# Kernel optimization log

Measured on AMD Instinct MI355X. Metric: run time of the kernel, lower is better.

## Reference

```python
import jax, jax.numpy as jnp
import numpy as np

DT = 0.1  # source sets dt = 0.1 globally
B, XS, SS, H = 128, 64, 16, 512  # batch, x_size, s_size, hidden_size


def setup_inputs() -> dict:
    key = jax.random.key(0)
    ks = jax.random.split(key, 14)
    sc = 1.0 / np.sqrt(H)  # PyTorch LSTM/Linear init bound
    u = lambda k, shape: jax.random.uniform(k, shape, jnp.float32, -sc, sc)
    return {
        "x": jax.random.normal(ks[0], (B, XS), jnp.float32),
        "s0": jax.random.normal(ks[1], (B, SS), jnp.float32),
        # LSTM layer 0 (input = x_size + s_size), gate order i,f,g,o
        "W_ih0": u(ks[2], (4 * H, XS + SS)),
        "W_hh0": u(ks[3], (4 * H, H)),
        "b_ih0": u(ks[4], (4 * H,)),
        "b_hh0": u(ks[5], (4 * H,)),
        # LSTM layer 1 (input = hidden)
        "W_ih1": u(ks[6], (4 * H, H)),
        "W_hh1": u(ks[7], (4 * H, H)),
        "b_ih1": u(ks[8], (4 * H,)),
        "b_hh1": u(ks[9], (4 * H,)),
        # fc: hidden -> s_size
        "W_fc": u(ks[10], (SS, H)),
        "b_fc": u(ks[11], (SS,)),
        "max_time": 20,
    }


def _lstm_cell(h, c, inp, W_ih, W_hh, b_ih, b_hh):
    g = inp @ W_ih.T + b_ih + h @ W_hh.T + b_hh  # [B, 4H]
    i, f, gg, o = jnp.split(g, 4, axis=-1)  # torch gate order i,f,g,o
    c = jax.nn.sigmoid(f) * c + jax.nn.sigmoid(i) * jnp.tanh(gg)
    h = jax.nn.sigmoid(o) * jnp.tanh(c)
    return h, c


def reference(x, s0, W_ih0, W_hh0, b_ih0, b_hh0, W_ih1, W_hh1, b_ih1, b_hh1, W_fc, b_fc, max_time):
    T = int(max_time / DT) + 1  # while cal_t <= max_time, cal_t += dt
    batch = x.shape[0]
    hid = W_hh0.shape[1]
    zeros = jnp.zeros((batch, hid), x.dtype)
    init = (zeros, zeros, zeros, zeros, s0)  # (h0,c0,h1,c1,current_s)

    def step(carry, _):
        h0, c0, h1, c1, s = carry
        inp = jnp.concatenate([x, s], axis=-1)  # [B, XS+SS]
        h0, c0 = _lstm_cell(h0, c0, inp, W_ih0, W_hh0, b_ih0, b_hh0)
        h1, c1 = _lstm_cell(h1, c1, h0, W_ih1, W_hh1, b_ih1, b_hh1)
        step_out = h1 @ W_fc.T + b_fc  # [B, SS] (dropout is identity in eval)
        s = s + step_out * DT  # residual Euler update
        return (h0, c0, h1, c1, s), (s, step_out)

    _, (outs, res) = jax.lax.scan(step, init, None, length=T)
    outputs = jnp.transpose(outs, (1, 0, 2))  # [B, T, SS]
    res_steps = jnp.transpose(res, (1, 0, 2))  # [B, T, SS]
    cal_times = jnp.arange(T, dtype=x.dtype) * DT
    return outputs, cal_times, res_steps
```

## Files before the change

### kernel.cpp

```cpp
#include <hip/hip_runtime.h>

#define NB    256
#define BT    1024
#define BATCH 128
#define HID   512
#define XSZ   64
#define SSZ   16
#define CPAD  32
#define SPIN_MAX (1 << 17)

typedef unsigned int uint;
typedef unsigned long long ulong64;
typedef _Float16 half2v __attribute__((ext_vector_type(2)));

#define AL8(p)    __hip_atomic_load((const ulong64*)(p), __ATOMIC_RELAXED, __HIP_MEMORY_SCOPE_AGENT)
#define AS4(p, v) __hip_atomic_store((uint*)(p), (v), __ATOMIC_RELAXED, __HIP_MEMORY_SCOPE_AGENT)

__device__ __align__(16) uint4 g_h0Q[2][64 * 128];
__device__ __align__(16) uint4 g_h1Q[2][64 * 128];
__device__ __align__(16) float g_Wcomb[4 * HID * HID];
__device__ int g_cnt[512 * CPAD];

__device__ __forceinline__ float sigf(float x) { return 1.f / (1.f + __expf(-x)); }
__device__ __forceinline__ float tanh_fast(float x) {
  float ax = fabsf(x); float e = __expf(-2.f * ax);
  return copysignf((1.f - e) / (1.f + e), x);
}
__device__ __forceinline__ uint pack_f16(float a, float b) {
  half2v h; h.x = (_Float16)a; h.y = (_Float16)b;
  return __builtin_bit_cast(uint, h);
}
__device__ __forceinline__ float2 up2(uint u) {
  half2v h = __builtin_bit_cast(half2v, u);
  return make_float2((float)h.x, (float)h.y);
}
__device__ __forceinline__ float fdot2(uint a, uint w, float c) {
#if __has_builtin(__builtin_amdgcn_fdot2)
  return __builtin_amdgcn_fdot2(__builtin_bit_cast(half2v, a),
                                __builtin_bit_cast(half2v, w), c, false);
#else
  float2 av = up2(a), wv = up2(w);
  return fmaf(av.x, wv.x, fmaf(av.y, wv.y, c));
#endif
}
__device__ __forceinline__ void dot8(uint a, uint4 w0, uint4 w1, float* acc) {
  acc[0] = fdot2(a, w0.x, acc[0]); acc[1] = fdot2(a, w0.y, acc[1]);
  acc[2] = fdot2(a, w0.z, acc[2]); acc[3] = fdot2(a, w0.w, acc[3]);
  acc[4] = fdot2(a, w1.x, acc[4]); acc[5] = fdot2(a, w1.y, acc[5]);
  acc[6] = fdot2(a, w1.z, acc[6]); acc[7] = fdot2(a, w1.w, acc[7]);
}
__device__ __forceinline__ void dots16(const uint4* __restrict__ apq,
                                       const uint*  __restrict__ wb,
                                       float* __restrict__ acc) {
  const ulong64* ap = (const ulong64*)apq;
  ulong64 lo[16], hi[16];
#pragma unroll
  for (int i = 0; i < 16; ++i) {
    lo[i] = AL8(ap + i * 256);
    hi[i] = AL8(ap + i * 256 + 1);
  }
#pragma unroll
  for (int i = 0; i < 16; ++i) {
    const uint4* w4 = (const uint4*)(wb + 32 * i);
    dot8((uint)lo[i],         w4[0], w4[1], acc);
    dot8((uint)(lo[i] >> 32), w4[2], w4[3], acc);
    dot8((uint)hi[i],         w4[4], w4[5], acc);
    dot8((uint)(hi[i] >> 32), w4[6], w4[7], acc);
  }
}

__device__ __forceinline__ void cnt_wait(int pid) {
  int guard = 0;
  while (__hip_atomic_load(&g_cnt[pid * CPAD], __ATOMIC_RELAXED, __HIP_MEMORY_SCOPE_AGENT) < NB) {
    __builtin_amdgcn_s_sleep(2);
    if (++guard > SPIN_MAX) break;
  }
  __builtin_amdgcn_sched_barrier(0);
}

__device__ __forceinline__ void group_wait(int pid, int pw, int tid, int* rel) {
  if ((tid >> 6) == pw) {
    cnt_wait(pid);
    if ((tid & 63) == 0)
      __hip_atomic_store(&rel[pid & 1], pid, __ATOMIC_RELEASE, __HIP_MEMORY_SCOPE_WORKGROUP);
  } else {
    int guard = 0;
    while (__hip_atomic_load(&rel[pid & 1], __ATOMIC_ACQUIRE, __HIP_MEMORY_SCOPE_WORKGROUP) < pid) {
      __builtin_amdgcn_s_sleep(1);
      if (++guard > SPIN_MAX) break;
    }
    __builtin_amdgcn_sched_barrier(0);
  }
}

__global__ void setup_kernel(float* __restrict__ out, int T) {
  int idx = blockIdx.x * blockDim.x + threadIdx.x;
  int n   = gridDim.x * blockDim.x;
  uint* z0 = (uint*)g_h0Q;
  uint* z1 = (uint*)g_h1Q;
  for (int i = idx; i < 2 * 64 * 128 * 4; i += n) { z0[i] = 0u; z1[i] = 0u; }
  for (int t = idx; t < T; t += n) out[BATCH * T * SSZ + t] = (float)t * 0.1f;
  for (int i = idx; i < 512 * CPAD; i += n) g_cnt[i] = 0;
}

__global__ void wcomb_kernel(const float* __restrict__ Wih0, const float* __restrict__ Wfc) {
  int idx = blockIdx.x * blockDim.x + threadIdx.x;
  int row = idx >> 9, k = idx & (HID - 1);
  float a = 0.f;
#pragma unroll
  for (int m = 0; m < SSZ; m++) a += Wih0[row * (XSZ + SSZ) + XSZ + m] * Wfc[m * HID + k];
  g_Wcomb[idx] = 0.1f * a;
}

__global__ __launch_bounds__(BT, 4) void persist_kernel(
    const float* __restrict__ x,    const float* __restrict__ s0,
    const float* __restrict__ Wih0, const float* __restrict__ Whh0,
    const float* __restrict__ bih0, const float* __restrict__ bhh0,
    const float* __restrict__ Wih1, const float* __restrict__ Whh1,
    const float* __restrict__ bih1, const float* __restrict__ bhh1,
    const float* __restrict__ Wfc,  const float* __restrict__ bfc,
    float* __restrict__ out, int T)
{
  __shared__ uint  lwT[4][256][8];
  __shared__ float gbuf[8][8][128];
  __shared__ float sbase[8][128];
  __shared__ float c0s[2][128], c1s[2][128];
  __shared__ uint  wfcP[16][268];
  __shared__ float b1s[8], ucs[8];
  __shared__ int   rel[2];

  const int bk  = blockIdx.x;
  const int tid = threadIdx.x;
  const int ks  = tid >> 7;
  const int b   = tid & 127;
  const int q0  = (ks & 3) * 16;
  const int kp0 = (ks & 3) * 64;

  if (tid == 0) { rel[0] = -1; rel[1] = -1; }

  for (int e = tid; e < 4 * 256 * 8; e += BT) {
    int mat = e >> 11, kp = (e >> 3) & 255, r = e & 7;
    int row = (r >> 1) * HID + 2 * bk + (r & 1);
    const float* src = (mat == 0) ? &Whh0[row * HID]
                     : (mat == 1) ? &g_Wcomb[row * HID]
                     : (mat == 2) ? &Wih1[row * HID] : &Whh1[row * HID];
    lwT[mat][kp][r] = pack_f16(src[2 * kp], src[2 * kp + 1]);
  }
  for (int e = tid; e < 16 * 256; e += BT) {
    int fs_ = e >> 8, kp = e & 255;
    wfcP[fs_][kp] = pack_f16(Wfc[fs_ * HID + 2 * kp], Wfc[fs_ * HID + 2 * kp + 1]);
  }
  {
    int r = tid >> 7, bb = tid & 127;
    int row = (r >> 1) * HID + 2 * bk + (r & 1);
    float a = bih0[row] + bhh0[row];
    const float* wr = Wih0 + row * (XSZ + SSZ);
#pragma unroll 4
    for (int k = 0; k < XSZ; k++) a = fmaf(wr[k], x[bb * XSZ + k], a);
    sbase[r][bb] = a;
  }
  if (tid < 8) {
    int row = (tid >> 1) * HID + 2 * bk + (tid & 1);
    b1s[tid] = bih1[row] + bhh1[row];
    float uc = 0.f;
    const float* ws = Wih0 + row * (XSZ + SSZ) + XSZ;
#pragma unroll
    for (int m = 0; m < SSZ; m++) uc = fmaf(ws[m], bfc[m], uc);
    ucs[tid] = 0.1f * uc;
  }
  __syncthreads();

  float u[8];
  if (tid < 128) {
#pragma unroll
    for (int r = 0; r < 8; r++) {
      int row = (r >> 1) * HID + 2 * bk + (r & 1);
      const float* ws = Wih0 + row * (XSZ + SSZ) + XSZ;
      float a = 0.f;
#pragma unroll
      for (int m = 0; m < SSZ; m++) a = fmaf(ws[m], s0[b * SSZ + m], a);
      u[r] = a - ucs[r];
    }
    c0s[0][b] = 0.f; c0s[1][b] = 0.f;
    c1s[0][b] = 0.f; c1s[1][b] = 0.f;
  }

  const bool fcw = (bk >= 128) && ((tid >> 6) == 15);
  const int  fb = bk - 128, lane = tid & 63, fs = lane & 15, fq = lane >> 4;
  float s_reg = 0.f, bfcj = 0.f;
  if (fcw && lane < SSZ) { s_reg = s0[fb * SSZ + lane]; bfcj = bfc[lane]; }

  auto fc_step = [&](int tt, const uint4* h1base) {
    const ulong64* hp = (const ulong64*)(h1base + fq * 16 * 128 + fb);
    ulong64 lo[16], hi[16];
#pragma unroll
    for (int i = 0; i < 16; ++i) {
      lo[i] = AL8(hp + i * 256);
      hi[i] = AL8(hp + i * 256 + 1);
    }
    const uint4* wp = (const uint4*)&wfcP[fs][fq * 64];
    float acc = 0.f;
#pragma unroll
    for (int i = 0; i < 16; ++i) {
      uint4 w = wp[i];
      acc = fdot2((uint)lo[i],         w.x, acc);
      acc = fdot2((uint)(lo[i] >> 32), w.y, acc);
      acc = fdot2((uint)hi[i],         w.z, acc);
      acc = fdot2((uint)(hi[i] >> 32), w.w, acc);
    }
    acc += __shfl_xor(acc, 16);
    acc += __shfl_xor(acc, 32);
    if (lane < SSZ) {
      float so = acc + bfcj;
      s_reg += 0.1f * so;
      out[fb * (T * SSZ) + tt * SSZ + fs] = s_reg;
      out[BATCH * T * SSZ + T + fb * (T * SSZ) + tt * SSZ + fs] = so;
    }
  };

  int p = 0;
  for (int t = 0; t < T; ++t) {
    if (ks >= 4 && t > 0) group_wait(2 * t, 8, tid, rel);
    {
      float acc[8] = {0, 0, 0, 0, 0, 0, 0, 0};
      const uint4* actQ = (ks < 4) ? g_h0Q[p] : g_h1Q[p];
      const uint*  wb   = &lwT[(ks < 4) ? 0 : 1][kp0][0];
      dots16(actQ + q0 * 128 + b, wb, acc);
#pragma unroll
      for (int r = 0; r < 8; r++) gbuf[ks][r][b] = acc[r];
    }
    __syncthreads();
    if (tid < 128) {
      float pre[8];
#pragma unroll
      for (int r = 0; r < 8; r++) {
        float s1 = gbuf[0][r][b] + gbuf[1][r][b] + gbuf[2][r][b] + gbuf[3][r][b];
        float s2 = gbuf[4][r][b] + gbuf[5][r][b] + gbuf[6][r][b] + gbuf[7][r][b];
        u[r] += s2 + ucs[r];
        pre[r] = sbase[r][b] + s1 + u[r];
      }
      float h[2];
#pragma unroll
      for (int jj = 0; jj < 2; jj++) {
        float c = c0s[jj][b];
        c = sigf(pre[2 + jj]) * c + sigf(pre[0 + jj]) * tanh_fast(pre[4 + jj]);
        c0s[jj][b] = c;
        h[jj] = sigf(pre[6 + jj]) * tanh_fast(c);
      }
      AS4(((uint*)&g_h0Q[p ^ 1][(bk >> 2) * 128 + b]) + (bk & 3), pack_f16(h[0], h[1]));
    }
    __syncthreads();
    if (tid == 0)
      __hip_atomic_fetch_add(&g_cnt[(2 * t + 1) * CPAD], 1, __ATOMIC_RELAXED, __HIP_MEMORY_SCOPE_AGENT);

    if (ks < 4) group_wait(2 * t + 1, 0, tid, rel);
    {
      float acc[8] = {0, 0, 0, 0, 0, 0, 0, 0};
      const uint4* actQ = (ks < 4) ? g_h0Q[p ^ 1] : g_h1Q[p];
      const uint*  wb   = &lwT[(ks < 4) ? 2 : 3][kp0][0];
      dots16(actQ + q0 * 128 + b, wb, acc);
#pragma unroll
      for (int r = 0; r < 8; r++) gbuf[ks][r][b] = acc[r];
    }
    if (fcw && t > 0) fc_step(t - 1, g_h1Q[p]);
    __syncthreads();
    if (tid < 128) {
      float pre[8];
#pragma unroll
      for (int r = 0; r < 8; r++) {
        float s1 = gbuf[0][r][b] + gbuf[1][r][b] + gbuf[2][r][b] + gbuf[3][r][b];
        float s2 = gbuf[4][r][b] + gbuf[5][r][b] + gbuf[6][r][b] + gbuf[7][r][b];
        pre[r] = b1s[r] + s1 + s2;
      }
      float h[2];
#pragma unroll
      for (int jj = 0; jj < 2; jj++) {
        float c = c1s[jj][b];
        c = sigf(pre[2 + jj]) * c + sigf(pre[0 + jj]) * tanh_fast(pre[4 + jj]);
        c1s[jj][b] = c;
        h[jj] = sigf(pre[6 + jj]) * tanh_fast(c);
      }
      AS4(((uint*)&g_h1Q[p ^ 1][(bk >> 2) * 128 + b]) + (bk & 3), pack_f16(h[0], h[1]));
    }
    __syncthreads();
    if (tid == 0)
      __hip_atomic_fetch_add(&g_cnt[(2 * t + 2) * CPAD], 1, __ATOMIC_RELAXED, __HIP_MEMORY_SCOPE_AGENT);
    p ^= 1;
  }

  if (fcw) {
    cnt_wait(2 * T);
    fc_step(T - 1, g_h1Q[p]);
  }
}

extern "C" void kernel_launch(void* const* d_in, const int* in_sizes, int n_in,
                              void* d_out, int out_size, void* d_ws, size_t ws_size,
                              hipStream_t stream) {
  const float* x    = (const float*)d_in[0];
  const float* s0   = (const float*)d_in[1];
  const float* Wih0 = (const float*)d_in[2];
  const float* Whh0 = (const float*)d_in[3];
  const float* bih0 = (const float*)d_in[4];
  const float* bhh0 = (const float*)d_in[5];
  const float* Wih1 = (const float*)d_in[6];
  const float* Whh1 = (const float*)d_in[7];
  const float* bih1 = (const float*)d_in[8];
  const float* bhh1 = (const float*)d_in[9];
  const float* Wfc  = (const float*)d_in[10];
  const float* bfc  = (const float*)d_in[11];
  float* out = (float*)d_out;

  const int T = out_size / (2 * BATCH * SSZ + 1);

  setup_kernel<<<64, 256, 0, stream>>>(out, T);
  wcomb_kernel<<<(4 * HID * HID) / 256, 256, 0, stream>>>(Wih0, Wfc);
  persist_kernel<<<NB, BT, 0, stream>>>(x, s0, Wih0, Whh0, bih0, bhh0,
                                        Wih1, Whh1, bih1, bhh1, Wfc, bfc, out, T);
}
```

Measured before the change: 4.707 ms.

## Restructure per-step work split and shard grid barrier counters across lanes

Rebalances the recurrent step so each warp group reads one activation vector once and does two matrix products with it. The h1 group computes the next layer-0 recurrent term and the layer-1 recurrent term together. The h0 group computes the layer-1 input term and the next step's layer-0 hidden term. This removes one activation load pass per phase and gives one phase entirely to the fc step. The single global arrival counter per phase is split into 8 padded counters. Each wave signals its own counter after a vmcnt drain, and waiters poll all 8 with a wave-wide __all to reduce atomic contention. It adds register pressure from the doubled accumulators and an extra shared buffer, and changes which gbuf slots carry which partial sums, which is correctness-sensitive.

After: 4.849 ms. 1.03x slower.

```diff
diff --git a/kernel.cpp b/kernel.cpp
--- a/kernel.cpp
+++ b/kernel.cpp
@@ -19,7 +19,7 @@
 __device__ __align__(16) uint4 g_h0Q[2][64 * 128];
 __device__ __align__(16) uint4 g_h1Q[2][64 * 128];
 __device__ __align__(16) float g_Wcomb[4 * HID * HID];
-__device__ int g_cnt[512 * CPAD];
+__device__ int g_cnt[512 * 8 * CPAD];
 
 __device__ __forceinline__ float sigf(float x) { return 1.f / (1.f + __expf(-x)); }
 __device__ __forceinline__ float tanh_fast(float x) {
@@ -49,9 +49,11 @@
   acc[4] = fdot2(a, w1.x, acc[4]); acc[5] = fdot2(a, w1.y, acc[5]);
   acc[6] = fdot2(a, w1.z, acc[6]); acc[7] = fdot2(a, w1.w, acc[7]);
 }
-__device__ __forceinline__ void dots16(const uint4* __restrict__ apq,
-                                       const uint*  __restrict__ wb,
-                                       float* __restrict__ acc) {
+__device__ __forceinline__ void dots16x2(const uint4* __restrict__ apq,
+                                         const uint*  __restrict__ wbA,
+                                         const uint*  __restrict__ wbB,
+                                         float* __restrict__ accA,
+                                         float* __restrict__ accB) {
   const ulong64* ap = (const ulong64*)apq;
   ulong64 lo[16], hi[16];
 #pragma unroll
@@ -61,18 +63,25 @@
   }
 #pragma unroll
   for (int i = 0; i < 16; ++i) {
-    const uint4* w4 = (const uint4*)(wb + 32 * i);
-    dot8((uint)lo[i],         w4[0], w4[1], acc);
-    dot8((uint)(lo[i] >> 32), w4[2], w4[3], acc);
-    dot8((uint)hi[i],         w4[4], w4[5], acc);
-    dot8((uint)(hi[i] >> 32), w4[6], w4[7], acc);
+    const uint4* wA = (const uint4*)(wbA + 32 * i);
+    const uint4* wB = (const uint4*)(wbB + 32 * i);
+    uint a0 = (uint)lo[i], a1 = (uint)(lo[i] >> 32);
+    uint a2 = (uint)hi[i], a3 = (uint)(hi[i] >> 32);
+    dot8(a0, wA[0], wA[1], accA); dot8(a0, wB[0], wB[1], accB);
+    dot8(a1, wA[2], wA[3], accA); dot8(a1, wB[2], wB[3], accB);
+    dot8(a2, wA[4], wA[5], accA); dot8(a2, wB[4], wB[5], accB);
+    dot8(a3, wA[6], wA[7], accA); dot8(a3, wB[6], wB[7], accB);
   }
 }
 
 __device__ __forceinline__ void cnt_wait(int pid) {
+  const int l = threadIdx.x & 63;
+  const int* cp = &g_cnt[(pid * 8 + (l & 7)) * CPAD];
   int guard = 0;
-  while (__hip_atomic_load(&g_cnt[pid * CPAD], __ATOMIC_RELAXED, __HIP_MEMORY_SCOPE_AGENT) < NB) {
-    __builtin_amdgcn_s_sleep(2);
+  for (;;) {
+    int v = __hip_atomic_load(cp, __ATOMIC_RELAXED, __HIP_MEMORY_SCOPE_AGENT);
+    if (__all(v >= 64)) break;
+    __builtin_amdgcn_s_sleep(1);
     if (++guard > SPIN_MAX) break;
   }
   __builtin_amdgcn_sched_barrier(0);
@@ -100,7 +109,7 @@
   uint* z1 = (uint*)g_h1Q;
   for (int i = idx; i < 2 * 64 * 128 * 4; i += n) { z0[i] = 0u; z1[i] = 0u; }
   for (int t = idx; t < T; t += n) out[BATCH * T * SSZ + t] = (float)t * 0.1f;
-  for (int i = idx; i < 512 * CPAD; i += n) g_cnt[i] = 0;
+  for (int i = idx; i < 512 * 8 * CPAD; i += n) g_cnt[i] = 0;
 }
 
 __global__ void wcomb_kernel(const float* __restrict__ Wih0, const float* __restrict__ Wfc) {
@@ -123,6 +132,7 @@
 {
   __shared__ uint  lwT[4][256][8];
   __shared__ float gbuf[8][8][128];
+  __shared__ float gbuf1[4][8][128];
   __shared__ float sbase[8][128];
   __shared__ float c0s[2][128], c1s[2][128];
   __shared__ uint  wfcP[16][268];
@@ -150,6 +160,7 @@
     int fs_ = e >> 8, kp = e & 255;
     wfcP[fs_][kp] = pack_f16(Wfc[fs_ * HID + 2 * kp], Wfc[fs_ * HID + 2 * kp + 1]);
   }
+  for (int e = tid; e < 4 * 8 * 128; e += BT) ((float*)gbuf)[e] = 0.f;
   {
     int r = tid >> 7, bb = tid & 127;
     int row = (r >> 1) * HID + 2 * bk + (r & 1);
@@ -220,14 +231,12 @@
 
   int p = 0;
   for (int t = 0; t < T; ++t) {
-    if (ks >= 4 && t > 0) group_wait(2 * t, 8, tid, rel);
-    {
-      float acc[8] = {0, 0, 0, 0, 0, 0, 0, 0};
-      const uint4* actQ = (ks < 4) ? g_h0Q[p] : g_h1Q[p];
-      const uint*  wb   = &lwT[(ks < 4) ? 0 : 1][kp0][0];
-      dots16(actQ + q0 * 128 + b, wb, acc);
-#pragma unroll
-      for (int r = 0; r < 8; r++) gbuf[ks][r][b] = acc[r];
+    if (ks >= 4) {
+      if (t > 0) group_wait(2 * t, 8, tid, rel);
+      float accA[8] = {0,0,0,0,0,0,0,0}, accB[8] = {0,0,0,0,0,0,0,0};
+      dots16x2(g_h1Q[p] + q0 * 128 + b, &lwT[1][kp0][0], &lwT[3][kp0][0], accA, accB);
+#pragma unroll
+      for (int r = 0; r < 8; r++) { gbuf[ks][r][b] = accA[r]; gbuf1[ks - 4][r][b] = accB[r]; }
     }
     __syncthreads();
     if (tid < 128) {
@@ -248,28 +257,28 @@
         h[jj] = sigf(pre[6 + jj]) * tanh_fast(c);
       }
       AS4(((uint*)&g_h0Q[p ^ 1][(bk >> 2) * 128 + b]) + (bk & 3), pack_f16(h[0], h[1]));
+      asm volatile("s_waitcnt vmcnt(0)" ::: "memory");
+      if ((tid & 63) == 0)
+        __hip_atomic_fetch_add(&g_cnt[((2 * t + 1) * 8 + (bk & 7)) * CPAD], 1,
+                               __ATOMIC_RELAXED, __HIP_MEMORY_SCOPE_AGENT);
     }
     __syncthreads();
-    if (tid == 0)
-      __hip_atomic_fetch_add(&g_cnt[(2 * t + 1) * CPAD], 1, __ATOMIC_RELAXED, __HIP_MEMORY_SCOPE_AGENT);
-
-    if (ks < 4) group_wait(2 * t + 1, 0, tid, rel);
-    {
-      float acc[8] = {0, 0, 0, 0, 0, 0, 0, 0};
-      const uint4* actQ = (ks < 4) ? g_h0Q[p ^ 1] : g_h1Q[p];
-      const uint*  wb   = &lwT[(ks < 4) ? 2 : 3][kp0][0];
-      dots16(actQ + q0 * 128 + b, wb, acc);
-#pragma unroll
-      for (int r = 0; r < 8; r++) gbuf[ks][r][b] = acc[r];
-    }
-    if (fcw && t > 0) fc_step(t - 1, g_h1Q[p]);
+    if (ks < 4) {
+      group_wait(2 * t + 1, 0, tid, rel);
+      float accA[8] = {0,0,0,0,0,0,0,0}, accB[8] = {0,0,0,0,0,0,0,0};
+      dots16x2(g_h0Q[p ^ 1] + q0 * 128 + b, &lwT[2][kp0][0], &lwT[0][kp0][0], accA, accB);
+#pragma unroll
+      for (int r = 0; r < 8; r++) { gbuf[4 + ks][r][b] = accA[r]; gbuf[ks][r][b] = accB[r]; }
+    } else {
+      if (fcw && t > 0) fc_step(t - 1, g_h1Q[p]);
+    }
     __syncthreads();
     if (tid < 128) {
       float pre[8];
 #pragma unroll
       for (int r = 0; r < 8; r++) {
-        float s1 = gbuf[0][r][b] + gbuf[1][r][b] + gbuf[2][r][b] + gbuf[3][r][b];
-        float s2 = gbuf[4][r][b] + gbuf[5][r][b] + gbuf[6][r][b] + gbuf[7][r][b];
+        float s1 = gbuf[4][r][b] + gbuf[5][r][b] + gbuf[6][r][b] + gbuf[7][r][b];
+        float s2 = gbuf1[0][r][b] + gbuf1[1][r][b] + gbuf1[2][r][b] + gbuf1[3][r][b];
         pre[r] = b1s[r] + s1 + s2;
       }
       float h[2];
@@ -281,10 +290,12 @@
         h[jj] = sigf(pre[6 + jj]) * tanh_fast(c);
       }
       AS4(((uint*)&g_h1Q[p ^ 1][(bk >> 2) * 128 + b]) + (bk & 3), pack_f16(h[0], h[1]));
+      asm volatile("s_waitcnt vmcnt(0)" ::: "memory");
+      if ((tid & 63) == 0)
+        __hip_atomic_fetch_add(&g_cnt[((2 * t + 2) * 8 + (bk & 7)) * CPAD], 1,
+                               __ATOMIC_RELAXED, __HIP_MEMORY_SCOPE_AGENT);
     }
     __syncthreads();
-    if (tid == 0)
-      __hip_atomic_fetch_add(&g_cnt[(2 * t + 2) * CPAD], 1, __ATOMIC_RELAXED, __HIP_MEMORY_SCOPE_AGENT);
     p ^= 1;
   }
 
```

## Split grid barrier into per-quarter counters so K-slices wait only on producers

Applied to the files above, without the earlier changes.

Replaces the single per-phase global counter, which waited for all 256 blocks, with four counters per phase, one per quarter of blocks (bk>>6). Each K-slice wave group now waits only for the quarter of blocks that produced the activation columns it reads, so consumers can start before the whole grid finishes. The per-block arrive now comes from two waves after an explicit vmcnt(0) wait, not from one thread after __syncthreads, to shorten the signal path. Tradeoffs are more counter memory and initialization, more spinning waves and more atomic traffic per step. Correctness depends on the store-then-atomic ordering holding under relaxed atomics.

Result: slower. 5.020 ms (+6.6%).

```diff
diff --git a/kernel.cpp b/kernel.cpp
--- a/kernel.cpp
+++ b/kernel.cpp
@@ -7,6 +7,7 @@
 #define XSZ   64
 #define SSZ   16
 #define CPAD  32
+#define QTGT  128
 #define SPIN_MAX (1 << 17)
 
 typedef unsigned int uint;
@@ -19,7 +20,7 @@
 __device__ __align__(16) uint4 g_h0Q[2][64 * 128];
 __device__ __align__(16) uint4 g_h1Q[2][64 * 128];
 __device__ __align__(16) float g_Wcomb[4 * HID * HID];
-__device__ int g_cnt[512 * CPAD];
+__device__ int g_cnt[2100 * 4 * CPAD];
 
 __device__ __forceinline__ float sigf(float x) { return 1.f / (1.f + __expf(-x)); }
 __device__ __forceinline__ float tanh_fast(float x) {
@@ -69,28 +70,23 @@
   }
 }
 
-__device__ __forceinline__ void cnt_wait(int pid) {
-  int guard = 0;
-  while (__hip_atomic_load(&g_cnt[pid * CPAD], __ATOMIC_RELAXED, __HIP_MEMORY_SCOPE_AGENT) < NB) {
-    __builtin_amdgcn_s_sleep(2);
-    if (++guard > SPIN_MAX) break;
-  }
-  __builtin_amdgcn_sched_barrier(0);
-}
-
-__device__ __forceinline__ void group_wait(int pid, int pw, int tid, int* rel) {
-  if ((tid >> 6) == pw) {
-    cnt_wait(pid);
-    if ((tid & 63) == 0)
-      __hip_atomic_store(&rel[pid & 1], pid, __ATOMIC_RELEASE, __HIP_MEMORY_SCOPE_WORKGROUP);
+__device__ __forceinline__ void quarter_wait(int pid, int ks, int tid, int* rel) {
+  const int line = (pid * 4 + (ks & 3)) * CPAD;
+  if (((tid >> 6) & 1) == 0) {
+    int guard = 0;
+    while (__hip_atomic_load(&g_cnt[line], __ATOMIC_RELAXED, __HIP_MEMORY_SCOPE_AGENT) < QTGT) {
+      __builtin_amdgcn_s_sleep(2);
+      if (++guard > SPIN_MAX) break;
+    }
+    __hip_atomic_store(&rel[ks], pid, __ATOMIC_RELEASE, __HIP_MEMORY_SCOPE_WORKGROUP);
   } else {
     int guard = 0;
-    while (__hip_atomic_load(&rel[pid & 1], __ATOMIC_ACQUIRE, __HIP_MEMORY_SCOPE_WORKGROUP) < pid) {
+    while (__hip_atomic_load(&rel[ks], __ATOMIC_ACQUIRE, __HIP_MEMORY_SCOPE_WORKGROUP) < pid) {
       __builtin_amdgcn_s_sleep(1);
       if (++guard > SPIN_MAX) break;
     }
-    __builtin_amdgcn_sched_barrier(0);
-  }
+  }
+  __builtin_amdgcn_sched_barrier(0);
 }
 
 __global__ void setup_kernel(float* __restrict__ out, int T) {
@@ -100,7 +96,8 @@
   uint* z1 = (uint*)g_h1Q;
   for (int i = idx; i < 2 * 64 * 128 * 4; i += n) { z0[i] = 0u; z1[i] = 0u; }
   for (int t = idx; t < T; t += n) out[BATCH * T * SSZ + t] = (float)t * 0.1f;
-  for (int i = idx; i < 512 * CPAD; i += n) g_cnt[i] = 0;
+  int ncnt = (2 * T + 2) * 4 * CPAD;
+  for (int i = idx; i < ncnt; i += n) g_cnt[i] = 0;
 }
 
 __global__ void wcomb_kernel(const float* __restrict__ Wih0, const float* __restrict__ Wfc) {
@@ -127,7 +124,7 @@
   __shared__ float c0s[2][128], c1s[2][128];
   __shared__ uint  wfcP[16][268];
   __shared__ float b1s[8], ucs[8];
-  __shared__ int   rel[2];
+  __shared__ int   rel[8];
 
   const int bk  = blockIdx.x;
   const int tid = threadIdx.x;
@@ -135,8 +132,9 @@
   const int b   = tid & 127;
   const int q0  = (ks & 3) * 16;
   const int kp0 = (ks & 3) * 64;
-
-  if (tid == 0) { rel[0] = -1; rel[1] = -1; }
+  const int myq = bk >> 6;
+
+  if (tid < 8) rel[tid] = -1;
 
   for (int e = tid; e < 4 * 256 * 8; e += BT) {
     int mat = e >> 11, kp = (e >> 3) & 255, r = e & 7;
@@ -220,7 +218,7 @@
 
   int p = 0;
   for (int t = 0; t < T; ++t) {
-    if (ks >= 4 && t > 0) group_wait(2 * t, 8, tid, rel);
+    if (ks >= 4 && t > 0) quarter_wait(2 * t, ks, tid, rel);
     {
       float acc[8] = {0, 0, 0, 0, 0, 0, 0, 0};
       const uint4* actQ = (ks < 4) ? g_h0Q[p] : g_h1Q[p];
@@ -248,12 +246,13 @@
         h[jj] = sigf(pre[6 + jj]) * tanh_fast(c);
       }
       AS4(((uint*)&g_h0Q[p ^ 1][(bk >> 2) * 128 + b]) + (bk & 3), pack_f16(h[0], h[1]));
+      asm volatile("s_waitcnt vmcnt(0)" ::: "memory");
+      if ((tid & 63) == 0)
+        __hip_atomic_fetch_add(&g_cnt[((2 * t + 1) * 4 + myq) * CPAD], 1,
+                               __ATOMIC_RELAXED, __HIP_MEMORY_SCOPE_AGENT);
     }
     __syncthreads();
-    if (tid == 0)
-      __hip_atomic_fetch_add(&g_cnt[(2 * t + 1) * CPAD], 1, __ATOMIC_RELAXED, __HIP_MEMORY_SCOPE_AGENT);
-
-    if (ks < 4) group_wait(2 * t + 1, 0, tid, rel);
+    if (ks < 4) quarter_wait(2 * t + 1, ks, tid, rel);
     {
       float acc[8] = {0, 0, 0, 0, 0, 0, 0, 0};
       const uint4* actQ = (ks < 4) ? g_h0Q[p ^ 1] : g_h1Q[p];
@@ -281,15 +280,25 @@
         h[jj] = sigf(pre[6 + jj]) * tanh_fast(c);
       }
       AS4(((uint*)&g_h1Q[p ^ 1][(bk >> 2) * 128 + b]) + (bk & 3), pack_f16(h[0], h[1]));
+      asm volatile("s_waitcnt vmcnt(0)" ::: "memory");
+      if ((tid & 63) == 0)
+        __hip_atomic_fetch_add(&g_cnt[((2 * t + 2) * 4 + myq) * CPAD], 1,
+                               __ATOMIC_RELAXED, __HIP_MEMORY_SCOPE_AGENT);
     }
     __syncthreads();
-    if (tid == 0)
-      __hip_atomic_fetch_add(&g_cnt[(2 * t + 2) * CPAD], 1, __ATOMIC_RELAXED, __HIP_MEMORY_SCOPE_AGENT);
     p ^= 1;
   }
 
   if (fcw) {
-    cnt_wait(2 * T);
+    for (int q = 0; q < 4; ++q) {
+      int guard = 0;
+      while (__hip_atomic_load(&g_cnt[(2 * T * 4 + q) * CPAD],
+                               __ATOMIC_RELAXED, __HIP_MEMORY_SCOPE_AGENT) < QTGT) {
+        __builtin_amdgcn_s_sleep(2);
+        if (++guard > SPIN_MAX) break;
+      }
+    }
+    __builtin_amdgcn_sched_barrier(0);
     fc_step(T - 1, g_h1Q[p]);
   }
 }
```

## Replace fdot2 gate matvecs with MFMA 16x16x32 and per-wave grid waits

Applied to the files above, without the earlier changes.

The per-step gate products move from packed fdot2 loops, where eight k-slices reduce through shared memory, to MFMA 16x16x32 f16 instructions. Each wave now computes a 16-batch tile over the full K, so only two partial buffers are summed. The block-level relay of the grid-barrier signal is dropped: every wave polls the global counter directly, and two waves per block increment it right after their stores. The fc step moves after the second barrier. The MFMA B operand is only half used (8 of 16 columns are zero-padded), and the number of pollers on the global counter grows.

Result: slower. 5.731 ms (+21.8%).

```diff
diff --git a/kernel.cpp b/kernel.cpp
--- a/kernel.cpp
+++ b/kernel.cpp
@@ -12,6 +12,8 @@
 typedef unsigned int uint;
 typedef unsigned long long ulong64;
 typedef _Float16 half2v __attribute__((ext_vector_type(2)));
+typedef _Float16 f16x8  __attribute__((ext_vector_type(8)));
+typedef float    f32x4  __attribute__((ext_vector_type(4)));
 
 #define AL8(p)    __hip_atomic_load((const ulong64*)(p), __ATOMIC_RELAXED, __HIP_MEMORY_SCOPE_AGENT)
 #define AS4(p, v) __hip_atomic_store((uint*)(p), (v), __ATOMIC_RELAXED, __HIP_MEMORY_SCOPE_AGENT)
@@ -43,54 +45,38 @@
   return fmaf(av.x, wv.x, fmaf(av.y, wv.y, c));
 #endif
 }
-__device__ __forceinline__ void dot8(uint a, uint4 w0, uint4 w1, float* acc) {
-  acc[0] = fdot2(a, w0.x, acc[0]); acc[1] = fdot2(a, w0.y, acc[1]);
-  acc[2] = fdot2(a, w0.z, acc[2]); acc[3] = fdot2(a, w0.w, acc[3]);
-  acc[4] = fdot2(a, w1.x, acc[4]); acc[5] = fdot2(a, w1.y, acc[5]);
-  acc[6] = fdot2(a, w1.z, acc[6]); acc[7] = fdot2(a, w1.w, acc[7]);
-}
-__device__ __forceinline__ void dots16(const uint4* __restrict__ apq,
-                                       const uint*  __restrict__ wb,
-                                       float* __restrict__ acc) {
-  const ulong64* ap = (const ulong64*)apq;
-  ulong64 lo[16], hi[16];
-#pragma unroll
-  for (int i = 0; i < 16; ++i) {
-    lo[i] = AL8(ap + i * 256);
-    hi[i] = AL8(ap + i * 256 + 1);
-  }
-#pragma unroll
-  for (int i = 0; i < 16; ++i) {
-    const uint4* w4 = (const uint4*)(wb + 32 * i);
-    dot8((uint)lo[i],         w4[0], w4[1], acc);
-    dot8((uint)(lo[i] >> 32), w4[2], w4[3], acc);
-    dot8((uint)hi[i],         w4[4], w4[5], acc);
-    dot8((uint)(hi[i] >> 32), w4[6], w4[7], acc);
-  }
-}
-
-__device__ __forceinline__ void cnt_wait(int pid) {
+
+__device__ __forceinline__ void mfma_pass(const uint4* __restrict__ actQ,
+                                          const uint4* __restrict__ wmat,
+                                          const uint4* __restrict__ zp,
+                                          int m0, int l15, int g, f32x4& acc) {
+  const ulong64* ap = (const ulong64*)(actQ + g * 128 + m0 + l15);
+  ulong64 lo[16], hh[16];
+#pragma unroll
+  for (int kt = 0; kt < 16; ++kt) {
+    lo[kt] = AL8(ap + kt * 1024);
+    hh[kt] = AL8(ap + kt * 1024 + 1);
+  }
+  const uint4* bp   = (l15 < 8) ? (wmat + g * 8 + l15) : zp;
+  const int    bstp = (l15 < 8) ? 32 : 0;
+#pragma unroll
+  for (int kt = 0; kt < 16; ++kt) {
+    uint4 av;
+    av.x = (uint)lo[kt]; av.y = (uint)(lo[kt] >> 32);
+    av.z = (uint)hh[kt]; av.w = (uint)(hh[kt] >> 32);
+    f16x8 a = __builtin_bit_cast(f16x8, av);
+    f16x8 b = __builtin_bit_cast(f16x8, bp[kt * bstp]);
+    acc = __builtin_amdgcn_mfma_f32_16x16x32_f16(a, b, acc, 0, 0, 0);
+  }
+}
+
+__device__ __forceinline__ void gwait(int pid) {
   int guard = 0;
-  while (__hip_atomic_load(&g_cnt[pid * CPAD], __ATOMIC_RELAXED, __HIP_MEMORY_SCOPE_AGENT) < NB) {
+  while (__hip_atomic_load(&g_cnt[pid * CPAD], __ATOMIC_RELAXED, __HIP_MEMORY_SCOPE_AGENT) < 2 * NB) {
     __builtin_amdgcn_s_sleep(2);
     if (++guard > SPIN_MAX) break;
   }
   __builtin_amdgcn_sched_barrier(0);
-}
-
-__device__ __forceinline__ void group_wait(int pid, int pw, int tid, int* rel) {
-  if ((tid >> 6) == pw) {
-    cnt_wait(pid);
-    if ((tid & 63) == 0)
-      __hip_atomic_store(&rel[pid & 1], pid, __ATOMIC_RELEASE, __HIP_MEMORY_SCOPE_WORKGROUP);
-  } else {
-    int guard = 0;
-    while (__hip_atomic_load(&rel[pid & 1], __ATOMIC_ACQUIRE, __HIP_MEMORY_SCOPE_WORKGROUP) < pid) {
-      __builtin_amdgcn_s_sleep(1);
-      if (++guard > SPIN_MAX) break;
-    }
-    __builtin_amdgcn_sched_barrier(0);
-  }
 }
 
 __global__ void setup_kernel(float* __restrict__ out, int T) {
@@ -121,43 +107,52 @@
     const float* __restrict__ Wfc,  const float* __restrict__ bfc,
     float* __restrict__ out, int T)
 {
-  __shared__ uint  lwT[4][256][8];
-  __shared__ float gbuf[8][8][128];
+  __shared__ uint4 lwM[4][16][4][8];
+  __shared__ uint4 zeroq;
+  __shared__ float gbuf[2][8][132];
   __shared__ float sbase[8][128];
+  __shared__ float u_s[8][128];
   __shared__ float c0s[2][128], c1s[2][128];
   __shared__ uint  wfcP[16][268];
   __shared__ float b1s[8], ucs[8];
-  __shared__ int   rel[2];
-
-  const int bk  = blockIdx.x;
-  const int tid = threadIdx.x;
-  const int ks  = tid >> 7;
-  const int b   = tid & 127;
-  const int q0  = (ks & 3) * 16;
-  const int kp0 = (ks & 3) * 64;
-
-  if (tid == 0) { rel[0] = -1; rel[1] = -1; }
-
-  for (int e = tid; e < 4 * 256 * 8; e += BT) {
-    int mat = e >> 11, kp = (e >> 3) & 255, r = e & 7;
-    int row = (r >> 1) * HID + 2 * bk + (r & 1);
+
+  const int bk   = blockIdx.x;
+  const int tid  = threadIdx.x;
+  const int wv   = tid >> 6;
+  const int lane = tid & 63;
+  const int l15  = lane & 15;
+  const int g    = lane >> 4;
+  const int m0   = (wv & 7) * 16;
+  const bool grp1 = (wv >= 8);
+
+  if (tid == 0) zeroq = make_uint4(0u, 0u, 0u, 0u);
+
+  for (int e = tid; e < 4 * 16 * 4 * 8; e += BT) {
+    int mat = e >> 9, kt = (e >> 5) & 15, gg = (e >> 3) & 3, nn = e & 7;
+    int row = (nn >> 1) * HID + 2 * bk + (nn & 1);
     const float* src = (mat == 0) ? &Whh0[row * HID]
                      : (mat == 1) ? &g_Wcomb[row * HID]
                      : (mat == 2) ? &Wih1[row * HID] : &Whh1[row * HID];
-    lwT[mat][kp][r] = pack_f16(src[2 * kp], src[2 * kp + 1]);
+    int k0 = kt * 32 + gg * 8;
+    uint4 v;
+    v.x = pack_f16(src[k0 + 0], src[k0 + 1]);
+    v.y = pack_f16(src[k0 + 2], src[k0 + 3]);
+    v.z = pack_f16(src[k0 + 4], src[k0 + 5]);
+    v.w = pack_f16(src[k0 + 6], src[k0 + 7]);
+    lwM[mat][kt][gg][nn] = v;
   }
   for (int e = tid; e < 16 * 256; e += BT) {
     int fs_ = e >> 8, kp = e & 255;
     wfcP[fs_][kp] = pack_f16(Wfc[fs_ * HID + 2 * kp], Wfc[fs_ * HID + 2 * kp + 1]);
   }
   {
-    int r = tid >> 7, bb = tid & 127;
+    int r = tid >> 7, bi = tid & 127;
     int row = (r >> 1) * HID + 2 * bk + (r & 1);
     float a = bih0[row] + bhh0[row];
     const float* wr = Wih0 + row * (XSZ + SSZ);
 #pragma unroll 4
-    for (int k = 0; k < XSZ; k++) a = fmaf(wr[k], x[bb * XSZ + k], a);
-    sbase[r][bb] = a;
+    for (int k = 0; k < XSZ; k++) a = fmaf(wr[k], x[bi * XSZ + k], a);
+    sbase[r][bi] = a;
   }
   if (tid < 8) {
     int row = (tid >> 1) * HID + 2 * bk + (tid & 1);
@@ -169,8 +164,6 @@
     ucs[tid] = 0.1f * uc;
   }
   __syncthreads();
-
-  float u[8];
   if (tid < 128) {
 #pragma unroll
     for (int r = 0; r < 8; r++) {
@@ -178,25 +171,26 @@
       const float* ws = Wih0 + row * (XSZ + SSZ) + XSZ;
       float a = 0.f;
 #pragma unroll
-      for (int m = 0; m < SSZ; m++) a = fmaf(ws[m], s0[b * SSZ + m], a);
-      u[r] = a - ucs[r];
-    }
-    c0s[0][b] = 0.f; c0s[1][b] = 0.f;
-    c1s[0][b] = 0.f; c1s[1][b] = 0.f;
-  }
-
-  const bool fcw = (bk >= 128) && ((tid >> 6) == 15);
-  const int  fb = bk - 128, lane = tid & 63, fs = lane & 15, fq = lane >> 4;
+      for (int m = 0; m < SSZ; m++) a = fmaf(ws[m], s0[tid * SSZ + m], a);
+      u_s[r][tid] = a - ucs[r];
+    }
+    c0s[0][tid] = 0.f; c0s[1][tid] = 0.f;
+    c1s[0][tid] = 0.f; c1s[1][tid] = 0.f;
+  }
+  __syncthreads();
+
+  const bool fcw = (bk >= 128) && (wv == 15);
+  const int  fb = bk - 128, fs = lane & 15, fq = lane >> 4;
   float s_reg = 0.f, bfcj = 0.f;
   if (fcw && lane < SSZ) { s_reg = s0[fb * SSZ + lane]; bfcj = bfc[lane]; }
 
   auto fc_step = [&](int tt, const uint4* h1base) {
     const ulong64* hp = (const ulong64*)(h1base + fq * 16 * 128 + fb);
-    ulong64 lo[16], hi[16];
+    ulong64 lo[16], hh[16];
 #pragma unroll
     for (int i = 0; i < 16; ++i) {
       lo[i] = AL8(hp + i * 256);
-      hi[i] = AL8(hp + i * 256 + 1);
+      hh[i] = AL8(hp + i * 256 + 1);
     }
     const uint4* wp = (const uint4*)&wfcP[fs][fq * 64];
     float acc = 0.f;
@@ -205,8 +199,8 @@
       uint4 w = wp[i];
       acc = fdot2((uint)lo[i],         w.x, acc);
       acc = fdot2((uint)(lo[i] >> 32), w.y, acc);
-      acc = fdot2((uint)hi[i],         w.z, acc);
-      acc = fdot2((uint)(hi[i] >> 32), w.w, acc);
+      acc = fdot2((uint)hh[i],         w.z, acc);
+      acc = fdot2((uint)(hh[i] >> 32), w.w, acc);
     }
     acc += __shfl_xor(acc, 16);
     acc += __shfl_xor(acc, 32);
@@ -220,24 +214,28 @@
 
   int p = 0;
   for (int t = 0; t < T; ++t) {
-    if (ks >= 4 && t > 0) group_wait(2 * t, 8, tid, rel);
+    if (grp1 && t > 0) gwait(2 * t);
     {
-      float acc[8] = {0, 0, 0, 0, 0, 0, 0, 0};
-      const uint4* actQ = (ks < 4) ? g_h0Q[p] : g_h1Q[p];
-      const uint*  wb   = &lwT[(ks < 4) ? 0 : 1][kp0][0];
-      dots16(actQ + q0 * 128 + b, wb, acc);
-#pragma unroll
-      for (int r = 0; r < 8; r++) gbuf[ks][r][b] = acc[r];
+      f32x4 acc = {0.f, 0.f, 0.f, 0.f};
+      const uint4* actQ = grp1 ? g_h1Q[p] : g_h0Q[p];
+      const uint4* wmat = &lwM[grp1 ? 1 : 0][0][0][0];
+      mfma_pass(actQ, wmat, &zeroq, m0, l15, g, acc);
+      if (l15 < 8) {
+#pragma unroll
+        for (int j = 0; j < 4; ++j) gbuf[grp1][l15][m0 + g * 4 + j] = acc[j];
+      }
     }
     __syncthreads();
     if (tid < 128) {
+      const int b = tid;
       float pre[8];
 #pragma unroll
       for (int r = 0; r < 8; r++) {
-        float s1 = gbuf[0][r][b] + gbuf[1][r][b] + gbuf[2][r][b] + gbuf[3][r][b];
-        float s2 = gbuf[4][r][b] + gbuf[5][r][b] + gbuf[6][r][b] + gbuf[7][r][b];
-        u[r] += s2 + ucs[r];
-        pre[r] = sbase[r][b] + s1 + u[r];
+        float s1 = gbuf[0][r][b];
+        float s2 = gbuf[1][r][b];
+        float uu = u_s[r][b] + s2 + ucs[r];
+        u_s[r][b] = uu;
+        pre[r] = sbase[r][b] + s1 + uu;
       }
       float h[2];
 #pragma unroll
@@ -248,30 +246,31 @@
         h[jj] = sigf(pre[6 + jj]) * tanh_fast(c);
       }
       AS4(((uint*)&g_h0Q[p ^ 1][(bk >> 2) * 128 + b]) + (bk & 3), pack_f16(h[0], h[1]));
+      asm volatile("s_waitcnt vmcnt(0)" ::: "memory");
+      if ((tid & 63) == 0)
+        __hip_atomic_fetch_add(&g_cnt[(2 * t + 1) * CPAD], 1,
+                               __ATOMIC_RELAXED, __HIP_MEMORY_SCOPE_AGENT);
     }
     __syncthreads();
-    if (tid == 0)
-      __hip_atomic_fetch_add(&g_cnt[(2 * t + 1) * CPAD], 1, __ATOMIC_RELAXED, __HIP_MEMORY_SCOPE_AGENT);
-
-    if (ks < 4) group_wait(2 * t + 1, 0, tid, rel);
+
+    if (!grp1) gwait(2 * t + 1);
     {
-      float acc[8] = {0, 0, 0, 0, 0, 0, 0, 0};
-      const uint4* actQ = (ks < 4) ? g_h0Q[p ^ 1] : g_h1Q[p];
-      const uint*  wb   = &lwT[(ks < 4) ? 2 : 3][kp0][0];
-      dots16(actQ + q0 * 128 + b, wb, acc);
-#pragma unroll
-      for (int r = 0; r < 8; r++) gbuf[ks][r][b] = acc[r];
-    }
-    if (fcw && t > 0) fc_step(t - 1, g_h1Q[p]);
+      f32x4 acc = {0.f, 0.f, 0.f, 0.f};
+      const uint4* actQ = grp1 ? g_h1Q[p] : g_h0Q[p ^ 1];
+      const uint4* wmat = &lwM[grp1 ? 3 : 2][0][0][0];
+      mfma_pass(actQ, wmat, &zeroq, m0, l15, g, acc);
+      if (l15 < 8) {
+#pragma unroll
+        for (int j = 0; j < 4; ++j) gbuf[grp1][l15][m0 + g * 4 + j] = acc[j];
+      }
+    }
     __syncthreads();
     if (tid < 128) {
+      const int b = tid;
       float pre[8];
 #pragma unroll
-      for (int r = 0; r < 8; r++) {
-        float s1 = gbuf[0][r][b] + gbuf[1][r][b] + gbuf[2][r][b] + gbuf[3][r][b];
-        float s2 = gbuf[4][r][b] + gbuf[5][r][b] + gbuf[6][r][b] + gbuf[7][r][b];
-        pre[r] = b1s[r] + s1 + s2;
-      }
+      for (int r = 0; r < 8; r++)
+        pre[r] = b1s[r] + gbuf[0][r][b] + gbuf[1][r][b];
       float h[2];
 #pragma unroll
       for (int jj = 0; jj < 2; jj++) {
@@ -281,15 +280,20 @@
         h[jj] = sigf(pre[6 + jj]) * tanh_fast(c);
       }
       AS4(((uint*)&g_h1Q[p ^ 1][(bk >> 2) * 128 + b]) + (bk & 3), pack_f16(h[0], h[1]));
+      asm volatile("s_waitcnt vmcnt(0)" ::: "memory");
+      if ((tid & 63) == 0)
+        __hip_atomic_fetch_add(&g_cnt[(2 * t + 2) * CPAD], 1,
+                               __ATOMIC_RELAXED, __HIP_MEMORY_SCOPE_AGENT);
     }
     __syncthreads();
-    if (tid == 0)
-      __hip_atomic_fetch_add(&g_cnt[(2 * t + 2) * CPAD], 1, __ATOMIC_RELAXED, __HIP_MEMORY_SCOPE_AGENT);
+
+    if (fcw && t > 0) fc_step(t - 1, g_h1Q[p]);
+
     p ^= 1;
   }
 
   if (fcw) {
-    cnt_wait(2 * T);
+    gwait(2 * T);
     fc_step(T - 1, g_h1Q[p]);
   }
 }
```
